# Optimization experiments

Measured on AMD Instinct MI355X. Metric: run time of the kernel, lower is better.

Reference implementation:

```python
import jax, jax.numpy as jnp
import numpy as np

HEAD_DIM = 64
N_HEADS = 32
LRPE_BASE = 512


def _rotate_half(x):
    x1, x2 = jnp.split(x, 2, axis=-1)
    return jnp.concatenate((-x2, x1), axis=-1)


def _cos_sin(L, dtype):
    inv_freq = 1.0 / (LRPE_BASE ** (jnp.arange(0, HEAD_DIM, 2, dtype=jnp.float32) / HEAD_DIM))
    t = jnp.arange(L, dtype=jnp.float32)
    freqs = t[:, None] * inv_freq[None, :]          # (L, hd/2)
    emb = jnp.concatenate((freqs, freqs), axis=-1)  # (L, hd)
    return jnp.cos(emb).astype(dtype), jnp.sin(emb).astype(dtype)


def setup_inputs() -> dict:
    key = jax.random.key(0)
    k1, k2, k3 = jax.random.split(key, 3)
    B, L, D = 2, 2048, 2048
    x = jax.random.normal(k1, (B, L, D), dtype=jnp.float32)
    wqkv = jax.random.normal(k2, (3 * D, D), dtype=jnp.float32) * (D ** -0.5)
    wo = jax.random.normal(k3, (D, D), dtype=jnp.float32) * (D ** -0.5)
    return {"x": x, "wqkv": wqkv, "wo": wo}


def reference(x, wqkv, wo):
    B, L, D = x.shape
    H, hd = N_HEADS, HEAD_DIM
    qkv = x @ wqkv.T                                   # (B, L, 3D)
    qkv = qkv.reshape(B, L, 3, H, hd)
    q, k, v = qkv[:, :, 0], qkv[:, :, 1], qkv[:, :, 2]  # (B, L, H, hd)

    cos, sin = _cos_sin(L, x.dtype)                    # (L, hd)
    cos = cos[None, :, None, :]
    sin = sin[None, :, None, :]
    q = q * cos + _rotate_half(q) * sin
    k = k * cos + _rotate_half(k) * sin

    scale = hd ** -0.5
    scores = jnp.einsum("bqhd,bkhd->bhqk", q, k) * scale  # (B, H, L, L)
    causal = jnp.triu(jnp.ones((L, L), dtype=bool), k=1)
    scores = jnp.where(causal[None, None], -jnp.inf, scores)
    attn = jax.nn.softmax(scores, axis=-1)
    out = jnp.einsum("bhqk,bkhd->bqhd", attn, v)       # (B, L, H, hd)
    out = out.reshape(B, L, D)
    return out @ wo.T
```

## Files before the change

kernel.cpp:

```cpp
#include <hip/hip_runtime.h>

using u16 = unsigned short;
using u32 = unsigned int;

typedef __attribute__((ext_vector_type(8))) __bf16 bf16x8;
typedef __attribute__((ext_vector_type(4))) __bf16 bf16x4;
typedef __attribute__((ext_vector_type(4))) float f32x4;

__device__ __forceinline__ u16 f2bf(float f) {
  u32 u = __builtin_bit_cast(u32, f);
  u = (u + 0x7fffu + ((u >> 16) & 1u)) >> 16;
  return (u16)u;
}
__device__ __forceinline__ float bf2f(u16 h) {
  u32 u = ((u32)h) << 16;
  return __builtin_bit_cast(float, u);
}

#if __has_builtin(__builtin_amdgcn_exp2f)
__device__ __forceinline__ float exp2_fast(float x) { return __builtin_amdgcn_exp2f(x); }
#else
__device__ __forceinline__ float exp2_fast(float x) {
  float r; asm("v_exp_f32 %0, %1" : "=v"(r) : "v"(x)); return r;
}
#endif

#define GLDS16(gp, lp)                                                              \
  __builtin_amdgcn_global_load_lds((const __attribute__((address_space(1))) void*)(gp), \
                                   (__attribute__((address_space(3))) void*)(lp), 16, 0, 0)

__global__ void cvt_kernel(const float* __restrict__ in, u16* __restrict__ out, int n4) {
  int idx = blockIdx.x * blockDim.x + threadIdx.x;
  int stride = gridDim.x * blockDim.x;
  for (int i = idx; i < n4; i += stride) {
    float4 f = ((const float4*)in)[i];
    ushort4 o;
    o.x = f2bf(f.x); o.y = f2bf(f.y); o.z = f2bf(f.z); o.w = f2bf(f.w);
    ((ushort4*)out)[i] = o;
  }
}

template <int OUT_BF16>
__global__ __launch_bounds__(256) void gemm_bt(const u16* __restrict__ A,
                                               const u16* __restrict__ B,
                                               void* __restrict__ Cv,
                                               int M, int N, int K) {
  __shared__ alignas(16) u16 As[128 * 32];
  __shared__ alignas(16) u16 Bs[128 * 32];
  const int tid = threadIdx.x;
  const int w = tid >> 6, lane = tid & 63;
  const int g = lane >> 4, lo = lane & 15;
  const int nwg = gridDim.x * gridDim.y;
  const int lid = blockIdx.y * gridDim.x + blockIdx.x;
  const int cpx = nwg >> 3;
  const int swz = (lid & 7) * cpx + (lid >> 3);
  const int bxs = swz % gridDim.x, bys = swz / gridDim.x;
  const int bm = bys * 128, bn = bxs * 128;
  const int wm = (w >> 1) * 64, wn = (w & 1) * 64;
  const int srow = lane >> 2;
  const int skp = (lane & 3) * 8;
  f32x4 acc[4][4] = {};

  for (int k0 = 0; k0 < K; k0 += 32) {
#pragma unroll
    for (int c2 = 0; c2 < 2; ++c2) {
      const int c = 2 * w + c2;
      const int row = c * 16 + srow;
      const u16* ga = A + (size_t)(bm + row) * K + k0 + skp;
      const u16* gb = B + (size_t)(bn + row) * K + k0 + skp;
      GLDS16(ga, As + c * 512);
      GLDS16(gb, Bs + c * 512);
    }
    __syncthreads();
    bf16x8 af[4], bfr[4];
#pragma unroll
    for (int i = 0; i < 4; ++i) {
      af[i] = *(const bf16x8*)(As + (wm + i * 16 + lo) * 32 + g * 8);
      bfr[i] = *(const bf16x8*)(Bs + (wn + i * 16 + lo) * 32 + g * 8);
    }
#pragma unroll
    for (int i = 0; i < 4; ++i)
#pragma unroll
      for (int j = 0; j < 4; ++j)
        acc[i][j] = __builtin_amdgcn_mfma_f32_16x16x32_bf16(af[i], bfr[j], acc[i][j], 0, 0, 0);
    __syncthreads();
  }

#pragma unroll
  for (int i = 0; i < 4; ++i) {
#pragma unroll
    for (int r = 0; r < 4; ++r) {
      const int row = bm + wm + i * 16 + g * 4 + r;
#pragma unroll
      for (int j = 0; j < 4; ++j) {
        const int col = bn + wn + j * 16 + lo;
        float v = acc[i][j][r];
        if (OUT_BF16)
          ((u16*)Cv)[(size_t)row * N + col] = f2bf(v);
        else
          ((float*)Cv)[(size_t)row * N + col] = v;
      }
    }
  }
}

__global__ __launch_bounds__(256) void rope_kernel(const u16* __restrict__ qkv,
                                                   u16* __restrict__ Q,
                                                   u16* __restrict__ Ko,
                                                   u16* __restrict__ VT) {
  const int bh = blockIdx.x;
  const int lt = blockIdx.y;
  const int b = bh >> 5, h = bh & 31;
  const int tid = threadIdx.x;
  const int l0 = lt * 64;
  const float QSC = 0.18033688011f;

  const int i = tid & 31;
  const float invf = exp2f(-(float)i * 0.28125f);
#pragma unroll
  for (int it = 0; it < 8; ++it) {
    const int l = (tid >> 5) + it * 8;
    const int m = b * 2048 + l0 + l;
    float s, c;
    __sincosf((float)(l0 + l) * invf, &s, &c);
    const int base = m * 6144 + h * 64 + i;
    float qlo = bf2f(qkv[base]), qhi = bf2f(qkv[base + 32]);
    float klo = bf2f(qkv[base + 2048]), khi = bf2f(qkv[base + 2048 + 32]);
    const int ob = (bh * 2048 + l0 + l) * 64 + i;
    Q[ob] = f2bf((qlo * c - qhi * s) * QSC);
    Q[ob + 32] = f2bf((qhi * c + qlo * s) * QSC);
    Ko[ob] = f2bf(klo * c - khi * s);
    Ko[ob + 32] = f2bf(khi * c + klo * s);
  }

  __shared__ alignas(16) u16 vs[64][72];
#pragma unroll
  for (int it = 0; it < 2; ++it) {
    const int c = tid * 2 + it;
    const int l = c >> 3, off = (c & 7) * 8;
    const int m = b * 2048 + l0 + l;
    *(uint4*)&vs[l][off] = *(const uint4*)&qkv[m * 6144 + 4096 + h * 64 + off];
  }
  __syncthreads();
#pragma unroll
  for (int it = 0; it < 2; ++it) {
    const int c = tid * 2 + it;
    const int d = c >> 3, lc = (c & 7) * 8;
    u32 w0 = (u32)vs[lc + 0][d] | ((u32)vs[lc + 1][d] << 16);
    u32 w1 = (u32)vs[lc + 2][d] | ((u32)vs[lc + 3][d] << 16);
    u32 w2 = (u32)vs[lc + 4][d] | ((u32)vs[lc + 5][d] << 16);
    u32 w3 = (u32)vs[lc + 6][d] | ((u32)vs[lc + 7][d] << 16);
    uint4 pk; pk.x = w0; pk.y = w1; pk.z = w2; pk.w = w3;
    *(uint4*)&VT[(size_t)(bh * 64 + d) * 2048 + l0 + lc] = pk;
  }
}

__global__ __launch_bounds__(256) void flash_kernel(const u16* __restrict__ Q,
                                                    const u16* __restrict__ K,
                                                    const u16* __restrict__ V,
                                                    u16* __restrict__ O) {
  __shared__ alignas(16) u16 KVs[2][2][64][64];
  __shared__ alignas(16) u16 Ps2[4][2][2][64][8];
  const int bid = blockIdx.x;
  const int xcd = bid & 7, slot = bid >> 3;
  const int bh = xcd * 8 + (slot & 7);
  const int pair = slot >> 3;
  const int b = bh >> 5, h = bh & 31;
  const int tid = threadIdx.x;
  const int w = tid >> 6, lane = tid & 63;
  const int g = lane >> 4, lo = lane & 15;
  const size_t bh2048 = (size_t)bh * 2048;
  const int srow = tid >> 3;
  const int sc8 = tid & 7;

  auto stage = [&](int buf, int kv0) {
#pragma unroll
    for (int p = 0; p < 2; ++p) {
      const int r = p * 32 + srow;
      const int col8 = sc8 ^ (r & 7);
      const u16* gk = K + (bh2048 + kv0 + r) * 64 + col8 * 8;
      const u16* gv = V + ((size_t)bh * 64 + r) * 2048 + kv0 + col8 * 8;
      u16* lbase = &KVs[buf][0][0][0] + p * 2048 + w * 512;
      GLDS16(gk, lbase);
      GLDS16(gv, lbase + 4096);
    }
  };

  for (int seg = 0; seg < 2; ++seg) {
    const int qt = seg ? 15 - pair : pair;
    const int qbase = qt * 128 + w * 32;
    const int ntile = 2 * qt + 2;

    bf16x8 qf[2][2];
#pragma unroll
    for (int qj = 0; qj < 2; ++qj)
#pragma unroll
      for (int ks = 0; ks < 2; ++ks)
        qf[qj][ks] = *(const bf16x8*)(Q + (bh2048 + qbase + qj * 16 + lo) * 64 + ks * 32 + g * 8);

    float mo[2] = {-1e30f, -1e30f};
    float ls[2] = {0.f, 0.f};
    f32x4 oacc[2][4] = {};

    stage(0, 0);
    __syncthreads();

    for (int t = 0; t < ntile; ++t) {
      const int cur = t & 1;
      const int kv0 = t * 64;
      if (t + 1 < ntile) stage(cur ^ 1, kv0 + 64);

      f32x4 st[4][2] = {};
#pragma unroll
      for (int kvi = 0; kvi < 4; ++kvi)
#pragma unroll
        for (int ks = 0; ks < 2; ++ks) {
          bf16x8 kf = *(const bf16x8*)&KVs[cur][0][kvi * 16 + lo][(ks * 32 + g * 8) ^ ((lo & 7) << 3)];
#pragma unroll
          for (int qj = 0; qj < 2; ++qj)
            st[kvi][qj] = __builtin_amdgcn_mfma_f32_16x16x32_bf16(kf, qf[qj][ks], st[kvi][qj], 0, 0, 0);
        }

      float corr2[2];
#pragma unroll
      for (int qj = 0; qj < 2; ++qj) {
        const int q = qbase + qj * 16 + lo;
        float tmax = -1e30f;
#pragma unroll
        for (int kvi = 0; kvi < 4; ++kvi)
#pragma unroll
          for (int r = 0; r < 4; ++r) {
            const int kv = kv0 + kvi * 16 + g * 4 + r;
            float s = st[kvi][qj][r];
            s = (kv <= q) ? s : -1e30f;
            st[kvi][qj][r] = s;
            tmax = fmaxf(tmax, s);
          }
        tmax = fmaxf(tmax, __shfl_xor(tmax, 16));
        tmax = fmaxf(tmax, __shfl_xor(tmax, 32));
        const float mn = fmaxf(mo[qj], tmax);
        const float corr = exp2_fast(mo[qj] - mn);
        mo[qj] = mn;
        float psum = 0.f;
#pragma unroll
        for (int kvi = 0; kvi < 4; ++kvi) {
          float p0 = exp2_fast(st[kvi][qj][0] - mn);
          float p1 = exp2_fast(st[kvi][qj][1] - mn);
          float p2 = exp2_fast(st[kvi][qj][2] - mn);
          float p3 = exp2_fast(st[kvi][qj][3] - mn);
          psum += (p0 + p1) + (p2 + p3);
          bf16x4 pk;
          pk[0] = (__bf16)p0; pk[1] = (__bf16)p1; pk[2] = (__bf16)p2; pk[3] = (__bf16)p3;
          *(bf16x4*)&Ps2[w][qj][kvi >> 1][((kvi & 1) * 2 + (g >> 1)) * 16 + lo][(g & 1) * 4] = pk;
        }
        psum += __shfl_xor(psum, 16);
        psum += __shfl_xor(psum, 32);
        ls[qj] = ls[qj] * corr + psum;
        corr2[qj] = corr;
      }

#pragma unroll
      for (int qi = 0; qi < 2; ++qi)
#pragma unroll
        for (int r = 0; r < 4; ++r) {
          const float cc = __shfl(corr2[qi], g * 4 + r);
#pragma unroll
          for (int ni = 0; ni < 4; ++ni) oacc[qi][ni][r] *= cc;
        }

      asm volatile("" ::: "memory");

      bf16x8 pa[2][2];
#pragma unroll
      for (int qi = 0; qi < 2; ++qi)
#pragma unroll
        for (int ks = 0; ks < 2; ++ks)
          pa[qi][ks] = *(const bf16x8*)&Ps2[w][qi][ks][lane][0];
#pragma unroll
      for (int ks = 0; ks < 2; ++ks)
#pragma unroll
        for (int ni = 0; ni < 4; ++ni) {
          bf16x8 vb = *(const bf16x8*)&KVs[cur][1][ni * 16 + lo][(ks * 32 + g * 8) ^ ((lo & 7) << 3)];
#pragma unroll
          for (int qi = 0; qi < 2; ++qi)
            oacc[qi][ni] = __builtin_amdgcn_mfma_f32_16x16x32_bf16(pa[qi][ks], vb, oacc[qi][ni], 0, 0, 0);
        }
      __syncthreads();
    }

#pragma unroll
    for (int qi = 0; qi < 2; ++qi) {
      const float linv = 1.0f / ls[qi];
#pragma unroll
      for (int r = 0; r < 4; ++r) {
        const float li = __shfl(linv, g * 4 + r);
        const int q = qbase + qi * 16 + g * 4 + r;
        const size_t rowoff = (size_t)(b * 2048 + q) * 2048 + h * 64;
#pragma unroll
        for (int ni = 0; ni < 4; ++ni)
          O[rowoff + ni * 16 + lo] = f2bf(oacc[qi][ni][r] * li);
      }
    }
  }
}

extern "C" void kernel_launch(void* const* d_in, const int* in_sizes, int n_in,
                              void* d_out, int out_size, void* d_ws, size_t ws_size,
                              hipStream_t stream) {
  const float* x = (const float*)d_in[0];
  const float* wqkv = (const float*)d_in[1];
  const float* wo = (const float*)d_in[2];
  float* out = (float*)d_out;

  u16* xb = (u16*)d_ws;
  u16* wqkvb = xb + (size_t)8388608;
  u16* wob = wqkvb + (size_t)12582912;
  u16* qkv = wob + (size_t)4194304;
  u16* qr = qkv + (size_t)25165824;
  u16* kr = qr + (size_t)8388608;
  u16* vt = kr + (size_t)8388608;
  u16* aout = xb;

  cvt_kernel<<<1024, 256, 0, stream>>>(x, xb, 8388608 / 4);
  cvt_kernel<<<1024, 256, 0, stream>>>(wqkv, wqkvb, 12582912 / 4);
  cvt_kernel<<<512, 256, 0, stream>>>(wo, wob, 4194304 / 4);

  gemm_bt<1><<<dim3(48, 32), 256, 0, stream>>>(xb, wqkvb, qkv, 4096, 6144, 2048);

  rope_kernel<<<dim3(64, 32), 256, 0, stream>>>(qkv, qr, kr, vt);

  flash_kernel<<<dim3(512), 256, 0, stream>>>(qr, kr, vt, aout);

  gemm_bt<0><<<dim3(16, 32), 256, 0, stream>>>(aout, wob, out, 4096, 2048, 2048);
}
```

Measured before the change: 440.8 us.

## Replace GEMM with 256x256-tile double-buffered, swizzled-LDS pipelined kernel

Replaces the simple 128x128-tile, single-buffered GEMM with a 512-thread kernel that computes 256x256 output tiles. It uses 64-wide K tiles staged in double-buffered dynamic LDS with an XOR swizzle. Loads for the next tile are interleaved with the MFMA phases, using explicit vmcnt waits, barriers and s_setprio, so global-to-LDS traffic overlaps with compute and each loaded element is reused more. The trade-offs are fewer workgroups, which leaves the out-projection grid small relative to the CU count, 128KB of LDS per block, and delicate hand-scheduled synchronisation. The exp2 helper is also simplified to always use inline asm.

```diff
diff --git a/kernel.cpp b/kernel.cpp
--- a/kernel.cpp
+++ b/kernel.cpp
@@ -17,13 +17,9 @@
   return __builtin_bit_cast(float, u);
 }
 
-#if __has_builtin(__builtin_amdgcn_exp2f)
-__device__ __forceinline__ float exp2_fast(float x) { return __builtin_amdgcn_exp2f(x); }
-#else
 __device__ __forceinline__ float exp2_fast(float x) {
   float r; asm("v_exp_f32 %0, %1" : "=v"(r) : "v"(x)); return r;
 }
-#endif
 
 #define GLDS16(gp, lp)                                                              \
   __builtin_amdgcn_global_load_lds((const __attribute__((address_space(1))) void*)(gp), \
@@ -41,67 +37,123 @@
 }
 
 template <int OUT_BF16>
-__global__ __launch_bounds__(256) void gemm_bt(const u16* __restrict__ A,
-                                               const u16* __restrict__ B,
-                                               void* __restrict__ Cv,
-                                               int M, int N, int K) {
-  __shared__ alignas(16) u16 As[128 * 32];
-  __shared__ alignas(16) u16 Bs[128 * 32];
+__global__ __launch_bounds__(512, 2) void gemm256(const u16* __restrict__ A,
+                                                  const u16* __restrict__ B,
+                                                  void* __restrict__ Cv,
+                                                  int M, int N, int K) {
+  extern __shared__ u16 lds[];
   const int tid = threadIdx.x;
   const int w = tid >> 6, lane = tid & 63;
   const int g = lane >> 4, lo = lane & 15;
+  const int wm = (w >> 2) * 128, wn = (w & 3) * 64;
   const int nwg = gridDim.x * gridDim.y;
   const int lid = blockIdx.y * gridDim.x + blockIdx.x;
   const int cpx = nwg >> 3;
   const int swz = (lid & 7) * cpx + (lid >> 3);
   const int bxs = swz % gridDim.x, bys = swz / gridDim.x;
-  const int bm = bys * 128, bn = bxs * 128;
-  const int wm = (w >> 1) * 64, wn = (w & 1) * 64;
-  const int srow = lane >> 2;
-  const int skp = (lane & 3) * 8;
-  f32x4 acc[4][4] = {};
-
-  for (int k0 = 0; k0 < K; k0 += 32) {
-#pragma unroll
-    for (int c2 = 0; c2 < 2; ++c2) {
-      const int c = 2 * w + c2;
-      const int row = c * 16 + srow;
-      const u16* ga = A + (size_t)(bm + row) * K + k0 + skp;
-      const u16* gb = B + (size_t)(bn + row) * K + k0 + skp;
-      GLDS16(ga, As + c * 512);
-      GLDS16(gb, Bs + c * 512);
-    }
-    __syncthreads();
-    bf16x8 af[4], bfr[4];
-#pragma unroll
-    for (int i = 0; i < 4; ++i) {
-      af[i] = *(const bf16x8*)(As + (wm + i * 16 + lo) * 32 + g * 8);
-      bfr[i] = *(const bf16x8*)(Bs + (wn + i * 16 + lo) * 32 + g * 8);
-    }
-#pragma unroll
-    for (int i = 0; i < 4; ++i)
-#pragma unroll
-      for (int j = 0; j < 4; ++j)
-        acc[i][j] = __builtin_amdgcn_mfma_f32_16x16x32_bf16(af[i], bfr[j], acc[i][j], 0, 0, 0);
-    __syncthreads();
-  }
-
-#pragma unroll
-  for (int i = 0; i < 4; ++i) {
+  const int bm = bys * 256, bn = bxs * 256;
+  const int NT = K >> 6;
+
+  auto stage_half = [&](int mat, int buf, int half, int kt) {
+    if (kt >= NT) return;
+    const u16* src = mat ? B : A;
+    const int rbase = (mat ? bn : bm) + half * 128;
+    u16* lbase0 = lds + mat * 32768 + buf * 16384 + half * 8192;
+#pragma unroll
+    for (int j = 0; j < 2; ++j) {
+      const int f = j * 512 + tid;
+      const int rl = f >> 3, cl = f & 7;
+      const int cg = cl ^ (rl & 7);
+      const u16* gp = src + (size_t)(rbase + rl) * K + kt * 64 + cg * 8;
+      GLDS16(gp, lbase0 + (j * 512 + w * 64) * 8);
+    }
+  };
+  auto lda = [&](int buf, int q, int m2, int ks) -> bf16x8 {
+    const int row = wm + q * 32 + m2 * 16 + lo;
+    const int cl = (ks * 4 + g) ^ (row & 7);
+    return *(const bf16x8*)(lds + buf * 16384 + row * 64 + cl * 8);
+  };
+  auto ldb = [&](int buf, int n, int ks) -> bf16x8 {
+    const int row = wn + n * 16 + lo;
+    const int cl = (ks * 4 + g) ^ (row & 7);
+    return *(const bf16x8*)(lds + 32768 + buf * 16384 + row * 64 + cl * 8);
+  };
+
+  f32x4 acc[8][4] = {};
+  bf16x8 bfrag[4][2];
+
+#define PHASE(buf, q, LDB, smat, sbuf, shalf, stile, vm)                                    \
+  do {                                                                                      \
+    bf16x8 af[2][2];                                                                        \
+    _Pragma("unroll") for (int m2_ = 0; m2_ < 2; ++m2_)                                     \
+    _Pragma("unroll") for (int ks_ = 0; ks_ < 2; ++ks_)                                     \
+      af[m2_][ks_] = lda(buf, q, m2_, ks_);                                                 \
+    if (LDB) {                                                                              \
+      _Pragma("unroll") for (int n_ = 0; n_ < 4; ++n_)                                      \
+      _Pragma("unroll") for (int ks_ = 0; ks_ < 2; ++ks_)                                   \
+        bfrag[n_][ks_] = ldb(buf, n_, ks_);                                                 \
+    }                                                                                       \
+    stage_half(smat, sbuf, shalf, stile);                                                   \
+    if ((vm) == 4) asm volatile("s_waitcnt vmcnt(4)");                                      \
+    else if ((vm) == 0) asm volatile("s_waitcnt vmcnt(0)");                                 \
+    __builtin_amdgcn_s_barrier();                                                           \
+    asm volatile("s_waitcnt lgkmcnt(0)");                                                   \
+    __builtin_amdgcn_sched_barrier(0);                                                      \
+    __builtin_amdgcn_s_setprio(1);                                                          \
+    _Pragma("unroll") for (int m2_ = 0; m2_ < 2; ++m2_)                                     \
+    _Pragma("unroll") for (int n_ = 0; n_ < 4; ++n_)                                        \
+    _Pragma("unroll") for (int ks_ = 0; ks_ < 2; ++ks_)                                     \
+      acc[(q) * 2 + m2_][n_] = __builtin_amdgcn_mfma_f32_16x16x32_bf16(                     \
+          af[m2_][ks_], bfrag[n_][ks_], acc[(q) * 2 + m2_][n_], 0, 0, 0);                   \
+    __builtin_amdgcn_s_setprio(0);                                                          \
+    __builtin_amdgcn_sched_barrier(0);                                                      \
+    __builtin_amdgcn_s_barrier();                                                           \
+  } while (0)
+
+  stage_half(1, 0, 0, 0); stage_half(1, 0, 1, 0);
+  stage_half(0, 0, 0, 0); stage_half(0, 0, 1, 0);
+  stage_half(1, 1, 0, 1); stage_half(1, 1, 1, 1);
+  asm volatile("s_waitcnt vmcnt(4)");
+  __builtin_amdgcn_s_barrier();
+
+  const int NITER = NT >> 1;
+  for (int i = 0; i < NITER - 1; ++i) {
+    const int to = 2 * i + 1, te = 2 * i + 2, tn = 2 * i + 3;
+    PHASE(0, 0, 1, 0, 1, 0, to, -1);
+    PHASE(0, 1, 0, 0, 1, 1, to, -1);
+    PHASE(0, 2, 0, 1, 0, 0, te, -1);
+    PHASE(0, 3, 0, 1, 0, 1, te, 4);
+    PHASE(1, 0, 1, 0, 0, 0, te, -1);
+    PHASE(1, 1, 0, 0, 0, 1, te, -1);
+    PHASE(1, 2, 0, 1, 1, 0, tn, -1);
+    PHASE(1, 3, 0, 1, 1, 1, tn, 4);
+  }
+  {
+    const int to = NT - 1;
+    PHASE(0, 0, 1, 0, 1, 0, to, -1);
+    PHASE(0, 1, 0, 0, 1, 1, to, -1);
+    PHASE(0, 2, 0, 1, 0, 0, NT, -1);
+    PHASE(0, 3, 0, 1, 0, 1, NT, 0);
+    PHASE(1, 0, 1, 0, 0, 0, NT, -1);
+    PHASE(1, 1, 0, 0, 0, 1, NT, -1);
+    PHASE(1, 2, 0, 1, 1, 0, NT, -1);
+    PHASE(1, 3, 0, 1, 1, 1, NT, -1);
+  }
+#undef PHASE
+
+#pragma unroll
+  for (int m = 0; m < 8; ++m)
 #pragma unroll
     for (int r = 0; r < 4; ++r) {
-      const int row = bm + wm + i * 16 + g * 4 + r;
-#pragma unroll
-      for (int j = 0; j < 4; ++j) {
-        const int col = bn + wn + j * 16 + lo;
-        float v = acc[i][j][r];
-        if (OUT_BF16)
-          ((u16*)Cv)[(size_t)row * N + col] = f2bf(v);
-        else
-          ((float*)Cv)[(size_t)row * N + col] = v;
+      const int row = bm + wm + m * 16 + g * 4 + r;
+#pragma unroll
+      for (int n = 0; n < 4; ++n) {
+        const int col = bn + wn + n * 16 + lo;
+        float v = acc[m][n][r];
+        if (OUT_BF16) ((u16*)Cv)[(size_t)row * N + col] = f2bf(v);
+        else ((float*)Cv)[(size_t)row * N + col] = v;
       }
     }
-  }
 }
 
 __global__ __launch_bounds__(256) void rope_kernel(const u16* __restrict__ qkv,
@@ -321,15 +373,18 @@
   u16* vt = kr + (size_t)8388608;
   u16* aout = xb;
 
+  hipFuncSetAttribute((const void*)gemm256<1>, hipFuncAttributeMaxDynamicSharedMemorySize, 131072);
+  hipFuncSetAttribute((const void*)gemm256<0>, hipFuncAttributeMaxDynamicSharedMemorySize, 131072);
+
   cvt_kernel<<<1024, 256, 0, stream>>>(x, xb, 8388608 / 4);
   cvt_kernel<<<1024, 256, 0, stream>>>(wqkv, wqkvb, 12582912 / 4);
   cvt_kernel<<<512, 256, 0, stream>>>(wo, wob, 4194304 / 4);
 
-  gemm_bt<1><<<dim3(48, 32), 256, 0, stream>>>(xb, wqkvb, qkv, 4096, 6144, 2048);
+  gemm256<1><<<dim3(24, 16), 512, 131072, stream>>>(xb, wqkvb, qkv, 4096, 6144, 2048);
 
   rope_kernel<<<dim3(64, 32), 256, 0, stream>>>(qkv, qr, kr, vt);
 
   flash_kernel<<<dim3(512), 256, 0, stream>>>(qr, kr, vt, aout);
 
-  gemm_bt<0><<<dim3(16, 32), 256, 0, stream>>>(aout, wob, out, 4096, 2048, 2048);
-}
+  gemm256<0><<<dim3(8, 16), 512, 131072, stream>>>(aout, wob, out, 4096, 2048, 2048);
+}
```

After: 403.7 us. -8.4%, faster.
